# Performance work log

Measured on AMD Instinct MI355X. Metric: run time of the kernel, lower is better.

## Reference

```python
import jax, jax.numpy as jnp
import numpy as np

B, T, V, H = 256, 512, 64, 256
IN = 2 * V + 1  # values + masks + delta_t = 129


def setup_inputs() -> dict:
    key = jax.random.key(0)
    ks = jax.random.split(key, 8)
    # sorted positive times with some entries zeroed (ragged padding -> t_exist False)
    t = jnp.sort(jax.random.uniform(ks[0], (B, T)), axis=1)
    keep = jax.random.uniform(ks[1], (B, T)) < 0.9
    times_in = jnp.where(keep, t, 0.0).astype(jnp.float32)
    data_in = jax.random.normal(ks[2], (B, T, V), dtype=jnp.float32)
    mask_in = (jax.random.uniform(ks[3], (B, T, V)) < 0.8).astype(jnp.float32)
    s = 1.0 / np.sqrt(H).astype(np.float32)
    W_ih = jax.random.uniform(ks[4], (3 * H, IN), minval=-s, maxval=s, dtype=jnp.float32)
    W_hh = jax.random.uniform(ks[5], (3 * H, H), minval=-s, maxval=s, dtype=jnp.float32)
    b_ih = jax.random.uniform(ks[6], (3 * H,), minval=-s, maxval=s, dtype=jnp.float32)
    b_hh = jax.random.uniform(ks[7], (3 * H,), minval=-s, maxval=s, dtype=jnp.float32)
    return {"times_in": times_in, "data_in": data_in, "mask_in": mask_in,
            "W_ih": W_ih, "W_hh": W_hh, "b_ih": b_ih, "b_hh": b_hh}


def reference(times_in, data_in, mask_in, W_ih, W_hh, b_ih, b_hh):
    b = times_in.shape[0]
    # delta_ts: times[:,1:] - times[:,:-1], padded with zero at the end
    delta = jnp.concatenate(
        [times_in[:, 1:] - times_in[:, :-1],
         jnp.zeros((b, 1), times_in.dtype)], axis=1)  # [B,T]
    # input_series = cat(values, masks, delta_t) -> [B,T,2V+1]
    x = jnp.concatenate([data_in, mask_in, delta[..., None]], axis=-1)
    t_exist = times_in > 0  # [B,T]
    h0 = jnp.zeros((b, W_hh.shape[1]), x.dtype)

    xs = (jnp.swapaxes(x, 0, 1), jnp.swapaxes(t_exist, 0, 1))  # time-major

    def step(h, inp):
        xt, m = inp  # xt: [B,IN], m: [B]
        gx = xt @ W_ih.T + b_ih  # [B,3H]
        gh = h @ W_hh.T + b_hh   # [B,3H]
        xr, xz, xn = jnp.split(gx, 3, axis=-1)
        hr, hz, hn = jnp.split(gh, 3, axis=-1)
        r = jax.nn.sigmoid(xr + hr)
        z = jax.nn.sigmoid(xz + hz)
        n = jnp.tanh(xn + r * hn)
        h_new = (1.0 - z) * n + z * h
        h = jnp.where(m[:, None], h_new, h)  # masked state carry
        return h, None

    h_final, _ = jax.lax.scan(step, h0, xs)
    return h_final
```

## Files before the change

kernel.cpp:

```cpp
#include <hip/hip_runtime.h>

#define Bn 256
#define Tn 512
#define Vn 64
#define Hn 256
#define INn 129
#define Cc 8
#define NCH (Tn / Cc)
#define WU 68
#define WSZ (768 * WU)
#define GX_OFF (262144)
#define GX_BYTES ((size_t)Bn * Tn * 768 * 2)
#define AST 168

typedef __fp16 half2_t __attribute__((ext_vector_type(2)));
typedef __fp16 half8_t __attribute__((ext_vector_type(8)));
typedef float f32x4 __attribute__((ext_vector_type(4)));

static __device__ __forceinline__ unsigned int cvt2(float a, float b) {
  return __builtin_bit_cast(unsigned int, __builtin_amdgcn_cvt_pkrtz(a, b));
}

static __device__ __forceinline__ float dot2(unsigned int w, unsigned int x, float acc) {
#if __has_builtin(__builtin_amdgcn_fdot2)
  return __builtin_amdgcn_fdot2(__builtin_bit_cast(half2_t, w),
                                __builtin_bit_cast(half2_t, x), acc, false);
#else
  half2_t a = __builtin_bit_cast(half2_t, w);
  half2_t b = __builtin_bit_cast(half2_t, x);
  return acc + (float)a.x * (float)b.x + (float)a.y * (float)b.y;
#endif
}

static __device__ __forceinline__ float xor1_add(float v) {
  int i = __builtin_bit_cast(int, v);
  int j = __builtin_amdgcn_ds_swizzle(i, 0x041F);
  return v + __builtin_bit_cast(float, j);
}

static __device__ __forceinline__ float fast_exp2(float x) {
#if __has_builtin(__builtin_amdgcn_exp2f)
  return __builtin_amdgcn_exp2f(x);
#else
  return exp2f(x);
#endif
}
static __device__ __forceinline__ float fast_rcp(float x) {
#if __has_builtin(__builtin_amdgcn_rcpf)
  return __builtin_amdgcn_rcpf(x);
#else
  return 1.f / x;
#endif
}
static __device__ __forceinline__ float sigmoid_f(float x) {
  return fast_rcp(1.f + fast_exp2(-1.44269504f * x));
}
static __device__ __forceinline__ float tanh_f(float x) {
  return 1.f - 2.f * fast_rcp(1.f + fast_exp2(2.88539008f * x));
}

__global__ void convert_wih(const float* __restrict__ W_ih, unsigned int* __restrict__ w16) {
  int idx = blockIdx.x * 256 + threadIdx.x;
  if (idx >= WSZ) return;
  int j = idx / WU, c = idx - j * WU;
  int col = 2 * c;
  float f0 = (col < INn) ? W_ih[(size_t)j * INn + col] : 0.f;
  float f1 = (col + 1 < INn) ? W_ih[(size_t)j * INn + col + 1] : 0.f;
  w16[idx] = cvt2(f0, f1);
}

__global__ __launch_bounds__(256, 4)
void gx_gemm(const float* __restrict__ times_in, const float* __restrict__ data_in,
             const float* __restrict__ mask_in, const unsigned int* __restrict__ w16,
             const float* __restrict__ b_ih, __fp16* __restrict__ gx) {
  __shared__ __align__(16) __fp16 xa[64 * AST];

  const int tid = threadIdx.x;
  const int bt = blockIdx.x;
  const int b = bt >> 3, tc = bt & 7;
  const int t0 = tc * 64;
  const int n0 = blockIdx.y * 256;

  {
    int r = tid >> 2, s = tid & 3;
    const float* src = (s < 2)
        ? data_in + ((size_t)b * Tn + t0 + r) * Vn + s * 32
        : mask_in + ((size_t)b * Tn + t0 + r) * Vn + (s - 2) * 32;
    unsigned int* dst = (unsigned int*)(xa + r * AST) + s * 16;
#pragma unroll
    for (int i = 0; i < 8; ++i) {
      float4 v = ((const float4*)src)[i];
      dst[2 * i] = cvt2(v.x, v.y);
      dst[2 * i + 1] = cvt2(v.z, v.w);
    }
  }
  if (tid < 64) {
    int g = t0 + tid;
    float tcur = times_in[(size_t)b * Tn + g];
    float d = (g < Tn - 1) ? times_in[(size_t)b * Tn + g + 1] - tcur : 0.f;
    unsigned int* p = (unsigned int*)(xa + tid * AST + 128);
    p[0] = cvt2(d, 0.f);
#pragma unroll
    for (int i = 1; i < 20; ++i) p[i] = 0u;
  }
  __syncthreads();

  const int w = tid >> 6, lane = tid & 63;
  const int m = lane & 15, q = lane >> 4;
  const int nw = n0 + w * 64;

  f32x4 acc[4][4];
#pragma unroll
  for (int i = 0; i < 4; ++i)
#pragma unroll
    for (int j = 0; j < 4; ++j) acc[i][j] = f32x4{0.f, 0.f, 0.f, 0.f};

#pragma unroll
  for (int kt = 0; kt < 5; ++kt) {
    const int k0 = kt * 32 + q * 8;
    half8_t bf[4], af[4];
#pragma unroll
    for (int nt = 0; nt < 4; ++nt) {
      int n = nw + nt * 16 + m;
      uint4 bv = *(const uint4*)(w16 + (size_t)n * WU + (k0 >> 1));
      bf[nt] = __builtin_bit_cast(half8_t, bv);
    }
#pragma unroll
    for (int mt = 0; mt < 4; ++mt) {
      uint4 av = *(const uint4*)(xa + (mt * 16 + m) * AST + k0);
      af[mt] = __builtin_bit_cast(half8_t, av);
    }
#pragma unroll
    for (int mt = 0; mt < 4; ++mt)
#pragma unroll
      for (int nt = 0; nt < 4; ++nt)
        acc[mt][nt] = __builtin_amdgcn_mfma_f32_16x16x32_f16(af[mt], bf[nt], acc[mt][nt], 0, 0, 0);
  }

  float bias[4];
#pragma unroll
  for (int nt = 0; nt < 4; ++nt) bias[nt] = b_ih[nw + nt * 16 + m];
#pragma unroll
  for (int mt = 0; mt < 4; ++mt) {
    int trow = t0 + mt * 16 + q * 4;
#pragma unroll
    for (int nt = 0; nt < 4; ++nt) {
      int n = nw + nt * 16 + m;
#pragma unroll
      for (int r = 0; r < 4; ++r) {
        gx[((size_t)b * Tn + trow + r) * 768 + n] = (__fp16)(acc[mt][nt][r] + bias[nt]);
      }
    }
  }
}

__global__ __launch_bounds__(512, 2)
void gru_scan2(const float* __restrict__ times_in, const float* __restrict__ W_hh,
               const float* __restrict__ b_hh, const __fp16* __restrict__ gx,
               float* __restrict__ out) {
  __shared__ __align__(16) __fp16 h_buf[2 * Hn];
  __shared__ __align__(16) float t_lds[Tn];

  const int tid = threadIdx.x;
  const int b = blockIdx.x;
  const int jg = tid >> 1;
  const int ks = tid & 1;

  t_lds[tid] = times_in[(size_t)b * Tn + tid];

  unsigned int whr[64], whz[64], whn[64];
  {
    const float* w0 = W_hh + (size_t)jg * Hn + ks * 128;
    const float* w1 = W_hh + (size_t)(jg + 256) * Hn + ks * 128;
    const float* w2 = W_hh + (size_t)(jg + 512) * Hn + ks * 128;
#pragma unroll
    for (int c = 0; c < 64; ++c) {
      whr[c] = cvt2(w0[2 * c], w0[2 * c + 1]);
      whz[c] = cvt2(w1[2 * c], w1[2 * c + 1]);
      whn[c] = cvt2(w2[2 * c], w2[2 * c + 1]);
    }
  }
  const float brh = b_hh[jg];
  const float bzh = b_hh[jg + 256];
  const float bhn = b_hh[jg + 512];

  h_buf[tid] = (__fp16)0.f;
  __syncthreads();

  const __fp16* gxb = gx + (size_t)b * Tn * 768;
  float hcur = 0.f;

  auto step = [&](int t, int curbuf, float gr, float gz, float gn) {
    float sr = 0.f, sz = 0.f, shn = 0.f;
    const uint4* hb = (const uint4*)(h_buf + curbuf * Hn + ks * 128);
#pragma unroll
    for (int c = 0; c < 16; ++c) {
      uint4 hv = hb[c];
      sr = dot2(whr[4 * c + 0], hv.x, sr);
      sz = dot2(whz[4 * c + 0], hv.x, sz);
      shn = dot2(whn[4 * c + 0], hv.x, shn);
      sr = dot2(whr[4 * c + 1], hv.y, sr);
      sz = dot2(whz[4 * c + 1], hv.y, sz);
      shn = dot2(whn[4 * c + 1], hv.y, shn);
      sr = dot2(whr[4 * c + 2], hv.z, sr);
      sz = dot2(whz[4 * c + 2], hv.z, sz);
      shn = dot2(whn[4 * c + 2], hv.z, shn);
      sr = dot2(whr[4 * c + 3], hv.w, sr);
      sz = dot2(whz[4 * c + 3], hv.w, sz);
      shn = dot2(whn[4 * c + 3], hv.w, shn);
    }
    sr = xor1_add(sr);
    sz = xor1_add(sz);
    shn = xor1_add(shn);
    float r = sigmoid_f(gr + sr + brh);
    float z = sigmoid_f(gz + sz + bzh);
    float n = tanh_f(gn + r * (shn + bhn));
    float hN = (1.f - z) * n + z * hcur;
    hcur = (t_lds[t] > 0.f) ? hN : hcur;
    if (ks == 0) h_buf[(curbuf ^ 1) * Hn + jg] = (__fp16)hcur;
    __syncthreads();
  };

  float g0r = (float)gxb[jg], g0z = (float)gxb[256 + jg], g0n = (float)gxb[512 + jg];
  float g1r = (float)gxb[768 + jg], g1z = (float)gxb[768 + 256 + jg],
        g1n = (float)gxb[768 + 512 + jg];

#pragma unroll 1
  for (int t = 0; t < Tn; t += 2) {
    __fp16 ar = (__fp16)0.f, az = (__fp16)0.f, an = (__fp16)0.f;
    __fp16 cr = (__fp16)0.f, cz = (__fp16)0.f, cn = (__fp16)0.f;
    if (t + 2 < Tn) {
      const __fp16* p = gxb + (size_t)(t + 2) * 768;
      ar = p[jg]; az = p[256 + jg]; an = p[512 + jg];
    }
    if (t + 3 < Tn) {
      const __fp16* p = gxb + (size_t)(t + 3) * 768;
      cr = p[jg]; cz = p[256 + jg]; cn = p[512 + jg];
    }
    step(t, 0, g0r, g0z, g0n);
    step(t + 1, 1, g1r, g1z, g1n);
    g0r = (float)ar; g0z = (float)az; g0n = (float)an;
    g1r = (float)cr; g1z = (float)cz; g1n = (float)cn;
  }

  if (ks == 0) out[(size_t)b * Hn + jg] = hcur;
}

template <bool USE_WS>
static __device__ __forceinline__ void phaseA_pass(int col, const unsigned int* __restrict__ w16,
                                                   const float* __restrict__ W_ih,
                                                   const unsigned int* x_lds, float* a) {
  const uint4* wp = (const uint4*)(w16) + (size_t)col * (WU / 4);
  const float* wf = W_ih + (size_t)col * INn;
#pragma unroll 2
  for (int kp = 0; kp < 8; ++kp) {
    uint4 wa, wb;
    if constexpr (USE_WS) {
      wa = wp[2 * kp];
      wb = wp[2 * kp + 1];
    } else {
      const float* f = wf + 16 * kp;
      wa.x = cvt2(f[0], f[1]);   wa.y = cvt2(f[2], f[3]);
      wa.z = cvt2(f[4], f[5]);   wa.w = cvt2(f[6], f[7]);
      wb.x = cvt2(f[8], f[9]);   wb.y = cvt2(f[10], f[11]);
      wb.z = cvt2(f[12], f[13]); wb.w = cvt2(f[14], f[15]);
    }
#pragma unroll
    for (int t = 0; t < Cc; ++t) {
      const uint4* xp = (const uint4*)&x_lds[t * WU + kp * 8];
      uint4 xa = xp[0], xb = xp[1];
      a[t] = dot2(wa.x, xa.x, a[t]);
      a[t] = dot2(wa.y, xa.y, a[t]);
      a[t] = dot2(wa.z, xa.z, a[t]);
      a[t] = dot2(wa.w, xa.w, a[t]);
      a[t] = dot2(wb.x, xb.x, a[t]);
      a[t] = dot2(wb.y, xb.y, a[t]);
      a[t] = dot2(wb.z, xb.z, a[t]);
      a[t] = dot2(wb.w, xb.w, a[t]);
    }
  }
  uint4 wt;
  if constexpr (USE_WS) {
    wt = wp[16];
  } else {
    wt.x = cvt2(wf[128], 0.f); wt.y = 0u; wt.z = 0u; wt.w = 0u;
  }
#pragma unroll
  for (int t = 0; t < Cc; ++t) {
    uint4 xt = *(const uint4*)&x_lds[t * WU + 64];
    a[t] = dot2(wt.x, xt.x, a[t]);
    a[t] = dot2(wt.y, xt.y, a[t]);
  }
}

template <bool USE_WS>
__global__ __launch_bounds__(512, 2)
void gru_scan_fb(const float* __restrict__ times_in, const float* __restrict__ data_in,
                 const float* __restrict__ mask_in, const unsigned int* __restrict__ w16,
                 const float* __restrict__ W_ih, const float* __restrict__ W_hh,
                 const float* __restrict__ b_ih, const float* __restrict__ b_hh,
                 float* __restrict__ out) {
  __shared__ __align__(16) float gx_lds[Cc * 768];
  __shared__ __align__(16) unsigned int x_lds[Cc * WU];
  __shared__ __align__(16) __fp16 h_buf[2 * Hn];
  __shared__ __align__(16) float t_lds[Tn];

  const int tid = threadIdx.x;
  const int b = blockIdx.x;
  const int jg = tid >> 1;
  const int ks = tid & 1;

  t_lds[tid] = times_in[(size_t)b * Tn + tid];

  unsigned int whr[64], whz[64], whn[64];
  {
    const float* w0 = W_hh + (size_t)jg * Hn + ks * 128;
    const float* w1 = W_hh + (size_t)(jg + 256) * Hn + ks * 128;
    const float* w2 = W_hh + (size_t)(jg + 512) * Hn + ks * 128;
#pragma unroll
    for (int c = 0; c < 64; ++c) {
      whr[c] = cvt2(w0[2 * c], w0[2 * c + 1]);
      whz[c] = cvt2(w1[2 * c], w1[2 * c + 1]);
      whn[c] = cvt2(w2[2 * c], w2[2 * c + 1]);
    }
  }
  const float brh = b_hh[jg];
  const float bzh = b_hh[jg + 256];
  const float bhn = b_hh[jg + 512];
  const float bi1 = b_ih[tid];
  const float bi2 = (tid < 256) ? b_ih[512 + tid] : 0.f;

  h_buf[tid] = (__fp16)0.f;
  __syncthreads();

  float hcur = 0.f;
  int cur = 0;
#pragma unroll 1
  for (int ch = 0; ch < NCH; ++ch) {
    const int t0 = ch * Cc;
    {
      int t = tid >> 6;
      int c = tid & 63;
      const float* src = (c < 32)
          ? data_in + ((size_t)b * Tn + t0 + t) * Vn + 2 * c
          : mask_in + ((size_t)b * Tn + t0 + t) * Vn + 2 * (c - 32);
      float2 v = *(const float2*)src;
      x_lds[t * WU + c] = cvt2(v.x, v.y);
      if (tid < Cc) {
        int g = t0 + tid;
        float d = (g < Tn - 1) ? (t_lds[g + 1] - t_lds[g]) : 0.f;
        uint4 tl;
        tl.x = cvt2(d, 0.f); tl.y = 0u; tl.z = 0u; tl.w = 0u;
        *(uint4*)&x_lds[tid * WU + 64] = tl;
      }
    }
    __syncthreads();
    {
      float a[Cc];
#pragma unroll
      for (int t = 0; t < Cc; ++t) a[t] = bi1;
      phaseA_pass<USE_WS>(tid, w16, W_ih, x_lds, a);
#pragma unroll
      for (int t = 0; t < Cc; ++t) gx_lds[t * 768 + tid] = a[t];
      if (tid < 256) {
#pragma unroll
        for (int t = 0; t < Cc; ++t) a[t] = bi2;
        phaseA_pass<USE_WS>(512 + tid, w16, W_ih, x_lds, a);
#pragma unroll
        for (int t = 0; t < Cc; ++t) gx_lds[t * 768 + 512 + tid] = a[t];
      }
    }
    __syncthreads();
    for (int tt = 0; tt < Cc; ++tt) {
      float sr = 0.f, sz = 0.f, shn = 0.f;
      const uint4* hb = (const uint4*)(h_buf + cur * Hn + ks * 128);
#pragma unroll
      for (int c = 0; c < 16; ++c) {
        uint4 hv = hb[c];
        sr = dot2(whr[4 * c + 0], hv.x, sr);
        sz = dot2(whz[4 * c + 0], hv.x, sz);
        shn = dot2(whn[4 * c + 0], hv.x, shn);
        sr = dot2(whr[4 * c + 1], hv.y, sr);
        sz = dot2(whz[4 * c + 1], hv.y, sz);
        shn = dot2(whn[4 * c + 1], hv.y, shn);
        sr = dot2(whr[4 * c + 2], hv.z, sr);
        sz = dot2(whz[4 * c + 2], hv.z, sz);
        shn = dot2(whn[4 * c + 2], hv.z, shn);
        sr = dot2(whr[4 * c + 3], hv.w, sr);
        sz = dot2(whz[4 * c + 3], hv.w, sz);
        shn = dot2(whn[4 * c + 3], hv.w, shn);
      }
      float gxr = gx_lds[tt * 768 + jg];
      float gxz = gx_lds[tt * 768 + 256 + jg];
      float gxn = gx_lds[tt * 768 + 512 + jg];
      sr = xor1_add(sr);
      sz = xor1_add(sz);
      shn = xor1_add(shn);
      float r = sigmoid_f(gxr + sr + brh);
      float z = sigmoid_f(gxz + sz + bzh);
      float n = tanh_f(gxn + r * (shn + bhn));
      float hN = (1.f - z) * n + z * hcur;
      hcur = (t_lds[t0 + tt] > 0.f) ? hN : hcur;
      if (ks == 0) h_buf[(cur ^ 1) * Hn + jg] = (__fp16)hcur;
      __syncthreads();
      cur ^= 1;
    }
  }
  if (ks == 0) out[(size_t)b * Hn + jg] = hcur;
}

extern "C" void kernel_launch(void* const* d_in, const int* in_sizes, int n_in,
                              void* d_out, int out_size, void* d_ws, size_t ws_size,
                              hipStream_t stream) {
  const float* times_in = (const float*)d_in[0];
  const float* data_in = (const float*)d_in[1];
  const float* mask_in = (const float*)d_in[2];
  const float* W_ih = (const float*)d_in[3];
  const float* W_hh = (const float*)d_in[4];
  const float* b_ih = (const float*)d_in[5];
  const float* b_hh = (const float*)d_in[6];
  float* out = (float*)d_out;

  unsigned int* w16 = (unsigned int*)d_ws;
  __fp16* gx = (__fp16*)((char*)d_ws + GX_OFF);

  if (ws_size >= GX_OFF + GX_BYTES) {
    hipLaunchKernelGGL(convert_wih, dim3((WSZ + 255) / 256), dim3(256), 0, stream, W_ih, w16);
    hipLaunchKernelGGL(gx_gemm, dim3(2048, 3), dim3(256), 0, stream,
                       times_in, data_in, mask_in, w16, b_ih, gx);
    hipLaunchKernelGGL(gru_scan2, dim3(Bn), dim3(512), 0, stream,
                       times_in, W_hh, b_hh, gx, out);
  } else if (ws_size >= (size_t)WSZ * 4) {
    hipLaunchKernelGGL(convert_wih, dim3((WSZ + 255) / 256), dim3(256), 0, stream, W_ih, w16);
    hipLaunchKernelGGL((gru_scan_fb<true>), dim3(Bn), dim3(512), 0, stream,
                       times_in, data_in, mask_in, w16, W_ih, W_hh, b_ih, b_hh, out);
  } else {
    hipLaunchKernelGGL((gru_scan_fb<false>), dim3(Bn), dim3(512), 0, stream,
                       times_in, data_in, mask_in, (const unsigned int*)nullptr, W_ih, W_hh,
                       b_ih, b_hh, out);
  }
}
```

Measured before the change: 797.4 us.

## Stage GEMM output through LDS, use DPP pair-sum, software-pipeline h loads

The gx_gemm epilogue now writes results into a shared-memory tile and then copies them out as coalesced 16-byte row stores, replacing scattered 2-byte global writes. The lane-pair reduction uses a DPP quad-permute instead of ds_swizzle, which avoids an LDS-unit round trip. The scan loop becomes a single-step loop that prefetches the next h_buf chunk inside the dot-product loop and preloads the next gx values and mask. The risks are extra LDS traffic and barriers in the GEMM epilogue, and higher register pressure in the scan.

```diff
diff --git a/kernel.cpp b/kernel.cpp
--- a/kernel.cpp
+++ b/kernel.cpp
@@ -12,6 +12,7 @@
 #define GX_OFF (262144)
 #define GX_BYTES ((size_t)Bn * Tn * 768 * 2)
 #define AST 168
+#define CST 264
 
 typedef __fp16 half2_t __attribute__((ext_vector_type(2)));
 typedef __fp16 half8_t __attribute__((ext_vector_type(8)));
@@ -32,10 +33,14 @@
 #endif
 }
 
-static __device__ __forceinline__ float xor1_add(float v) {
-  int i = __builtin_bit_cast(int, v);
-  int j = __builtin_amdgcn_ds_swizzle(i, 0x041F);
+static __device__ __forceinline__ float pair_sum(float v) {
+#if __has_builtin(__builtin_amdgcn_update_dpp)
+  int x = __builtin_amdgcn_update_dpp(0, __builtin_bit_cast(int, v), 0xB1, 0xF, 0xF, true);
+  return v + __builtin_bit_cast(float, x);
+#else
+  int j = __builtin_amdgcn_ds_swizzle(__builtin_bit_cast(int, v), 0x041F);
   return v + __builtin_bit_cast(float, j);
+#endif
 }
 
 static __device__ __forceinline__ float fast_exp2(float x) {
@@ -73,7 +78,9 @@
 void gx_gemm(const float* __restrict__ times_in, const float* __restrict__ data_in,
              const float* __restrict__ mask_in, const unsigned int* __restrict__ w16,
              const float* __restrict__ b_ih, __fp16* __restrict__ gx) {
-  __shared__ __align__(16) __fp16 xa[64 * AST];
+  __shared__ __align__(16) char raw[64 * CST * 2];
+  __fp16* xa = (__fp16*)raw;
+  __fp16* ct = (__fp16*)raw;
 
   const int tid = threadIdx.x;
   const int bt = blockIdx.x;
@@ -140,17 +147,24 @@
   float bias[4];
 #pragma unroll
   for (int nt = 0; nt < 4; ++nt) bias[nt] = b_ih[nw + nt * 16 + m];
-#pragma unroll
-  for (int mt = 0; mt < 4; ++mt) {
-    int trow = t0 + mt * 16 + q * 4;
-#pragma unroll
-    for (int nt = 0; nt < 4; ++nt) {
-      int n = nw + nt * 16 + m;
-#pragma unroll
-      for (int r = 0; r < 4; ++r) {
-        gx[((size_t)b * Tn + trow + r) * 768 + n] = (__fp16)(acc[mt][nt][r] + bias[nt]);
-      }
-    }
+
+  __syncthreads();
+#pragma unroll
+  for (int mt = 0; mt < 4; ++mt)
+#pragma unroll
+    for (int nt = 0; nt < 4; ++nt)
+#pragma unroll
+      for (int r = 0; r < 4; ++r)
+        ct[(mt * 16 + q * 4 + r) * CST + w * 64 + nt * 16 + m] =
+            (__fp16)(acc[mt][nt][r] + bias[nt]);
+  __syncthreads();
+
+  {
+    const int tt = tid >> 2, qq = tid & 3;
+    const uint4* src = (const uint4*)(ct + tt * CST) + qq * 8;
+    uint4* dst = (uint4*)(gx + ((size_t)b * Tn + t0 + tt) * 768 + n0) + qq * 8;
+#pragma unroll
+    for (int i = 0; i < 8; ++i) dst[i] = src[i];
   }
 }
 
@@ -190,57 +204,70 @@
   const __fp16* gxb = gx + (size_t)b * Tn * 768;
   float hcur = 0.f;
 
-  auto step = [&](int t, int curbuf, float gr, float gz, float gn) {
+  float gr = (float)gxb[jg], gz = (float)gxb[256 + jg], gn = (float)gxb[512 + jg];
+  float mt = t_lds[0];
+
+#pragma unroll 1
+  for (int t = 0; t < Tn; ++t) {
+    __fp16 pr = (__fp16)0.f, pz = (__fp16)0.f, pn = (__fp16)0.f;
+    float mtn = 0.f;
+    if (t + 1 < Tn) {
+      const __fp16* p = gxb + (size_t)(t + 1) * 768;
+      pr = p[jg]; pz = p[256 + jg]; pn = p[512 + jg];
+      mtn = t_lds[t + 1];
+    }
+
+    const int cur = t & 1;
+    const uint4* hb = (const uint4*)(h_buf + cur * Hn) + ks * 16;
+
     float sr = 0.f, sz = 0.f, shn = 0.f;
-    const uint4* hb = (const uint4*)(h_buf + curbuf * Hn + ks * 128);
-#pragma unroll
-    for (int c = 0; c < 16; ++c) {
-      uint4 hv = hb[c];
-      sr = dot2(whr[4 * c + 0], hv.x, sr);
-      sz = dot2(whz[4 * c + 0], hv.x, sz);
-      shn = dot2(whn[4 * c + 0], hv.x, shn);
-      sr = dot2(whr[4 * c + 1], hv.y, sr);
-      sz = dot2(whz[4 * c + 1], hv.y, sz);
-      shn = dot2(whn[4 * c + 1], hv.y, shn);
-      sr = dot2(whr[4 * c + 2], hv.z, sr);
-      sz = dot2(whz[4 * c + 2], hv.z, sz);
-      shn = dot2(whn[4 * c + 2], hv.z, shn);
-      sr = dot2(whr[4 * c + 3], hv.w, sr);
-      sz = dot2(whz[4 * c + 3], hv.w, sz);
-      shn = dot2(whn[4 * c + 3], hv.w, shn);
-    }
-    sr = xor1_add(sr);
-    sz = xor1_add(sz);
-    shn = xor1_add(shn);
+    uint4 p0 = hb[0], p1 = hb[1];
+#pragma unroll
+    for (int cc = 0; cc < 8; ++cc) {
+      uint4 q0 = p0, q1 = p1;
+      if (cc < 7) { q0 = hb[2 * cc + 2]; q1 = hb[2 * cc + 3]; }
+      const int cb = cc * 8;
+      sr = dot2(whr[cb + 0], p0.x, sr);
+      sz = dot2(whz[cb + 0], p0.x, sz);
+      shn = dot2(whn[cb + 0], p0.x, shn);
+      sr = dot2(whr[cb + 1], p0.y, sr);
+      sz = dot2(whz[cb + 1], p0.y, sz);
+      shn = dot2(whn[cb + 1], p0.y, shn);
+      sr = dot2(whr[cb + 2], p0.z, sr);
+      sz = dot2(whz[cb + 2], p0.z, sz);
+      shn = dot2(whn[cb + 2], p0.z, shn);
+      sr = dot2(whr[cb + 3], p0.w, sr);
+      sz = dot2(whz[cb + 3], p0.w, sz);
+      shn = dot2(whn[cb + 3], p0.w, shn);
+      sr = dot2(whr[cb + 4], p1.x, sr);
+      sz = dot2(whz[cb + 4], p1.x, sz);
+      shn = dot2(whn[cb + 4], p1.x, shn);
+      sr = dot2(whr[cb + 5], p1.y, sr);
+      sz = dot2(whz[cb + 5], p1.y, sz);
+      shn = dot2(whn[cb + 5], p1.y, shn);
+      sr = dot2(whr[cb + 6], p1.z, sr);
+      sz = dot2(whz[cb + 6], p1.z, sz);
+      shn = dot2(whn[cb + 6], p1.z, shn);
+      sr = dot2(whr[cb + 7], p1.w, sr);
+      sz = dot2(whz[cb + 7], p1.w, sz);
+      shn = dot2(whn[cb + 7], p1.w, shn);
+      p0 = q0; p1 = q1;
+    }
+
+    sr = pair_sum(sr);
+    sz = pair_sum(sz);
+    shn = pair_sum(shn);
+
     float r = sigmoid_f(gr + sr + brh);
     float z = sigmoid_f(gz + sz + bzh);
     float n = tanh_f(gn + r * (shn + bhn));
     float hN = (1.f - z) * n + z * hcur;
-    hcur = (t_lds[t] > 0.f) ? hN : hcur;
-    if (ks == 0) h_buf[(curbuf ^ 1) * Hn + jg] = (__fp16)hcur;
+    hcur = (mt > 0.f) ? hN : hcur;
+
+    if (ks == 0) h_buf[(cur ^ 1) * Hn + jg] = (__fp16)hcur;
     __syncthreads();
-  };
-
-  float g0r = (float)gxb[jg], g0z = (float)gxb[256 + jg], g0n = (float)gxb[512 + jg];
-  float g1r = (float)gxb[768 + jg], g1z = (float)gxb[768 + 256 + jg],
-        g1n = (float)gxb[768 + 512 + jg];
-
-#pragma unroll 1
-  for (int t = 0; t < Tn; t += 2) {
-    __fp16 ar = (__fp16)0.f, az = (__fp16)0.f, an = (__fp16)0.f;
-    __fp16 cr = (__fp16)0.f, cz = (__fp16)0.f, cn = (__fp16)0.f;
-    if (t + 2 < Tn) {
-      const __fp16* p = gxb + (size_t)(t + 2) * 768;
-      ar = p[jg]; az = p[256 + jg]; an = p[512 + jg];
-    }
-    if (t + 3 < Tn) {
-      const __fp16* p = gxb + (size_t)(t + 3) * 768;
-      cr = p[jg]; cz = p[256 + jg]; cn = p[512 + jg];
-    }
-    step(t, 0, g0r, g0z, g0n);
-    step(t + 1, 1, g1r, g1z, g1n);
-    g0r = (float)ar; g0z = (float)az; g0n = (float)an;
-    g1r = (float)cr; g1z = (float)cz; g1n = (float)cn;
+
+    gr = (float)pr; gz = (float)pz; gn = (float)pn; mt = mtn;
   }
 
   if (ks == 0) out[(size_t)b * Hn + jg] = hcur;
@@ -393,9 +420,9 @@
       float gxr = gx_lds[tt * 768 + jg];
       float gxz = gx_lds[tt * 768 + 256 + jg];
       float gxn = gx_lds[tt * 768 + 512 + jg];
-      sr = xor1_add(sr);
-      sz = xor1_add(sz);
-      shn = xor1_add(shn);
+      sr = pair_sum(sr);
+      sz = pair_sum(sz);
+      shn = pair_sum(shn);
       float r = sigmoid_f(gxr + sr + brh);
       float z = sigmoid_f(gxz + sz + bzh);
       float n = tanh_f(gxn + r * (shn + bhn));
```

New measurement: 781.5 us. -2.0%, faster.
